# Kernel optimization log

Hardware: AMD Instinct MI355X
Metric: run time of the kernel (lower is better)

The kernel has to match this reference:

```python
import jax, jax.numpy as jnp
import numpy as np
import math

IN_C, OUT_C, KH, KW = 128, 128, 3, 3
GROUPS_NUM, NUM_W = 8, 8
STRIDE, PAD, DIL = 1, 1, 1
BETA = 1.0


def setup_inputs() -> dict:
    key = jax.random.key(0)
    ks = jax.random.split(key, 6)
    B, H, W = 8, 56, 56
    n = IN_C * KH * KW
    bound = math.sqrt(6.0 / n)  # reset_parameters bound for weight templates
    inputs = jax.random.normal(ks[0], (B, IN_C, H, W), jnp.float32)
    mask = jax.random.randint(ks[1], (B, H, W), 0, GROUPS_NUM)
    Alpha = jax.random.uniform(ks[2], (B, GROUPS_NUM, H, W), jnp.float32)
    weight_templates = jax.random.uniform(ks[3], (OUT_C * IN_C * KH * KW, NUM_W), jnp.float32, -bound, bound)
    routing_w = jax.random.normal(ks[4], (GROUPS_NUM * NUM_W, IN_C), jnp.float32) * 0.01
    routing_b = jnp.zeros((GROUPS_NUM * NUM_W,), jnp.float32)
    bias = jnp.zeros((OUT_C,), jnp.float32)
    return dict(inputs=inputs, mask=mask, Alpha=Alpha, weight_templates=weight_templates,
                routing_w=routing_w, routing_b=routing_b, bias=bias, use_alpha=1)


def _unfold(x):
    # torch F.unfold-compatible im2col: [B, C*KH*KW, Ho, Wo], channel-major feature order
    return jax.lax.conv_general_dilated_patches(
        x, (KH, KW), (STRIDE, STRIDE), [(PAD, PAD), (PAD, PAD)],
        rhs_dilation=(DIL, DIL), dimension_numbers=('NCHW', 'OIHW', 'NCHW'))


def reference(inputs, mask, Alpha, weight_templates, routing_w, routing_b, bias, use_alpha):
    B, C, H, W = inputs.shape
    K = IN_C * KH * KW
    # SE-style routing: GAP -> fc -> scaled sigmoid (alpha=1.0 in source)
    x_se = inputs.reshape(B, C, -1).mean(-1)                              # [B, C]
    x_se = 2.0 * jax.nn.sigmoid(x_se @ routing_w.T + routing_b) / NUM_W   # [B, G*num_W]
    # blend weight templates: F.linear(x_se.reshape(-1,num_W), weight)
    w = x_se.reshape(B * GROUPS_NUM, NUM_W) @ weight_templates.T          # [B*G, O*K]
    w = w.reshape(B, GROUPS_NUM, OUT_C, K).transpose(0, 2, 3, 1)          # [B, O, K, G]
    patches = _unfold(inputs)                                             # [B, K, Ho, Wo]
    # per-group convolution outputs, then per-pixel group routing
    y = jnp.einsum('bokg,bkhw->boghw', w, patches)                        # [B, O, G, Ho, Wo]
    if use_alpha:
        probs = jax.nn.softmax(BETA * Alpha, axis=1)                      # soft routing [B, G, Ho, Wo]
    else:
        probs = jax.nn.one_hot(mask, GROUPS_NUM, axis=1, dtype=y.dtype)   # hard per-pixel group select
    out = jnp.einsum('boghw,bghw->bohw', y, probs)
    return out + bias.reshape(1, -1, 1, 1)
```

## Files before the change

kernel.cpp:

```cpp
#include <hip/hip_runtime.h>
#include <stdint.h>

#define IN_C   128
#define OUT_C  128
#define KTOT   1152
#define NG     8
#define NW     8
#define NB     8
#define HH     56
#define WWID   56
#define NPIX   3136
#define PPAD   3200
#define MTOT   1024
#define HALO   58
#define HPIX   (HALO*HALO)


typedef __attribute__((ext_vector_type(8))) short short8;
typedef __attribute__((ext_vector_type(8))) unsigned short ushort8;
typedef __attribute__((ext_vector_type(4))) float f32x4;

__device__ __forceinline__ unsigned short f2bf(float f) {
    unsigned u = __float_as_uint(f);
    u += 0x7FFF + ((u >> 16) & 1);
    return (unsigned short)(u >> 16);
}

__device__ __forceinline__ void cp16(const unsigned short* g, unsigned short* l) {
    __builtin_amdgcn_global_load_lds(
        (const __attribute__((address_space(1))) unsigned int*)g,
        (__attribute__((address_space(3))) unsigned int*)l,
        16, 0, 0);
}

__global__ __launch_bounds__(256) void gap_kernel(const float* __restrict__ in,
                                                  float* __restrict__ xse) {
    const int bc = blockIdx.x;
    const float* src = in + (size_t)bc * NPIX;
    float s = 0.f;
    for (int i = threadIdx.x; i < NPIX / 4; i += 256) {
        float4 v = ((const float4*)src)[i];
        s += v.x + v.y + v.z + v.w;
    }
    #pragma unroll
    for (int off = 32; off; off >>= 1) s += __shfl_down(s, off);
    __shared__ float ws4[4];
    if ((threadIdx.x & 63) == 0) ws4[threadIdx.x >> 6] = s;
    __syncthreads();
    if (threadIdx.x == 0)
        xse[bc] = (ws4[0] + ws4[1] + ws4[2] + ws4[3]) * (1.0f / (float)NPIX);
}

__global__ __launch_bounds__(64) void route_kernel(const float* __restrict__ xse,
                                                   const float* __restrict__ rw,
                                                   const float* __restrict__ rb,
                                                   float* __restrict__ r) {
    const int b = blockIdx.x;
    const int gj = threadIdx.x;
    __shared__ float xs[IN_C];
    xs[gj] = xse[b * IN_C + gj];
    xs[gj + 64] = xse[b * IN_C + 64 + gj];
    __syncthreads();
    float acc = rb[gj];
    #pragma unroll 8
    for (int c = 0; c < IN_C; c++) acc += xs[c] * rw[gj * IN_C + c];
    r[b * 64 + gj] = 0.25f / (1.0f + expf(-acc));
}

__global__ __launch_bounds__(256) void tconv_kernel(const float* __restrict__ T,
                                                    unsigned short* __restrict__ Abf) {
    const int id = blockIdx.x * 256 + threadIdx.x;
    const int m = id / 144;
    const int kc = id - m * 144;
    const int o = m >> 3, j = m & 7;
    const int s = kc >> 4;
    const int c0 = (kc & 15) << 3;
    ushort8 v;
    #pragma unroll
    for (int i = 0; i < 8; i++)
        v[i] = f2bf(T[((size_t)(o * KTOT + (c0 + i) * 9 + s)) * 8 + j]);
    *(ushort8*)&Abf[(size_t)m * KTOT + s * 128 + c0] = v;
}

__global__ __launch_bounds__(256) void transpose_kernel(const float* __restrict__ in,
                                                        unsigned short* __restrict__ Xt) {
    __shared__ unsigned short tile[128 * 128];
    const int t  = threadIdx.x;
    const int yt = blockIdx.x;
    const int b  = blockIdx.y;
    const int y0 = yt * 2;

    #pragma unroll
    for (int it = 0; it < 14; it++) {
        const int f = it * 256 + t;
        const int c = f / 28;
        const int rem = f - c * 28;
        const int y = rem / 14;
        const int x4 = rem - y * 14;
        const float4 v = *(const float4*)(in + ((size_t)(b * IN_C + c)) * NPIX
                                          + (y0 + y) * WWID + x4 * 4);
        unsigned short bf0 = f2bf(v.x), bf1 = f2bf(v.y), bf2 = f2bf(v.z), bf3 = f2bf(v.w);
        const int ppb = (y * WWID + x4 * 4) ^ (((c >> 3) & 15) << 2);
        uint2 pk;
        pk.x = (unsigned)bf0 | ((unsigned)bf1 << 16);
        pk.y = (unsigned)bf2 | ((unsigned)bf3 << 16);
        *(uint2*)&tile[c * 128 + ppb] = pk;
    }
    __syncthreads();

    #pragma unroll
    for (int it = 0; it < 7; it++) {
        const int ch = it * 256 + t;
        const int oct = ch & 15;
        const int pp = ch >> 4;
        const int sw = oct << 2;
        ushort8 v;
        #pragma unroll
        for (int i = 0; i < 8; i++)
            v[i] = tile[(oct * 8 + i) * 128 + (pp ^ sw)];
        const int y2 = (pp >= WWID) ? 1 : 0;
        const int xg = pp - y2 * WWID;
        const size_t hp = (size_t)b * HPIX + (y0 + y2 + 1) * HALO + (xg + 1);
        *(ushort8*)&Xt[hp * 128 + oct * 8] = v;
    }

    if (t < 64) {
        const int pi = t >> 4, oct = t & 15;
        const int yy = y0 + 1 + (pi >> 1);
        const int xx = (pi & 1) * 57;
        *(ushort8*)&Xt[((size_t)b * HPIX + yy * HALO + xx) * 128 + oct * 8] =
            (ushort8){0, 0, 0, 0, 0, 0, 0, 0};
    }
    if (yt == 0 || yt == 27) {
        const int yy = (yt == 0) ? 0 : 57;
        #pragma unroll
        for (int it = 0; it < 4; it++) {
            const int ch = it * 256 + t;
            if (ch < 928) {
                const int xx = ch >> 4, oct = ch & 15;
                *(ushort8*)&Xt[((size_t)b * HPIX + yy * HALO + xx) * 128 + oct * 8] =
                    (ushort8){0, 0, 0, 0, 0, 0, 0, 0};
            }
        }
    }
}

__global__ __launch_bounds__(256) void s_kernel(const float* __restrict__ Alpha,
                                                const int* __restrict__ mask,
                                                const float* __restrict__ r,
                                                const int* __restrict__ use_alpha,
                                                float* __restrict__ Sws) {
    const int b = blockIdx.y;
    const int p = blockIdx.x * 256 + threadIdx.x;
    __shared__ float rsh[64];
    if (threadIdx.x < 64) rsh[threadIdx.x] = r[b * 64 + threadIdx.x];
    __syncthreads();
    if (p >= PPAD) return;
    float sj[8] = {0, 0, 0, 0, 0, 0, 0, 0};
    if (p < NPIX) {
        float pr[8];
        if (use_alpha[0]) {
            float a[8], m = -1e30f;
            #pragma unroll
            for (int g = 0; g < 8; g++) {
                a[g] = Alpha[((size_t)(b * NG + g)) * NPIX + p];
                m = fmaxf(m, a[g]);
            }
            float sum = 0.f;
            #pragma unroll
            for (int g = 0; g < 8; g++) { pr[g] = expf(a[g] - m); sum += pr[g]; }
            float inv = 1.f / sum;
            #pragma unroll
            for (int g = 0; g < 8; g++) pr[g] *= inv;
        } else {
            int mg = mask[(size_t)b * NPIX + p];
            #pragma unroll
            for (int g = 0; g < 8; g++) pr[g] = (g == mg) ? 1.f : 0.f;
        }
        #pragma unroll
        for (int g = 0; g < 8; g++)
            #pragma unroll
            for (int j = 0; j < 8; j++) sj[j] += pr[g] * rsh[g * 8 + j];
    }
    float* dst = Sws + ((size_t)b * PPAD + p) * 8;
    *(f32x4*)dst = (f32x4){sj[0], sj[1], sj[2], sj[3]};
    *(f32x4*)(dst + 4) = (f32x4){sj[4], sj[5], sj[6], sj[7]};
}

__global__ __launch_bounds__(256) void gemm_kernel(const unsigned short* __restrict__ Abf,
                                                   const unsigned short* __restrict__ Xt,
                                                   const float* __restrict__ Sws,
                                                   const float* __restrict__ bias,
                                                   float* __restrict__ out) {
    __shared__ __align__(16) unsigned short Ash[2][512 * 8];
    __shared__ __align__(16) unsigned short Bsh[2][512 * 8];
    const int tid = threadIdx.x;
    const int wv = tid >> 6, ln = tid & 63;
    const int lq = ln >> 4, lr = ln & 15;
    const int wrow = wv >> 1, wcol = wv & 1;

    const int lid = blockIdx.x;
    const int b   = lid & 7;
    const int sl  = lid >> 3;
    const int mt  = sl & 7;
    const int nt  = sl >> 3;

    f32x4 acc[4][4];
    #pragma unroll
    for (int i = 0; i < 4; i++)
        #pragma unroll
        for (int j = 0; j < 4; j++) acc[i][j] = (f32x4){0.f, 0.f, 0.f, 0.f};

    const int r0 = tid >> 2,  q0 = (tid & 3) ^ (r0 & 3);
    const int r1 = r0 + 64,   q1 = (tid & 3) ^ (r1 & 3);
    const unsigned short* ga0 = Abf + (size_t)(mt * 128 + r0) * KTOT + q0 * 8;
    const unsigned short* ga1 = Abf + (size_t)(mt * 128 + r1) * KTOT + q1 * 8;
    const int p0 = min(nt * 128 + r0, NPIX - 1);
    const int p1 = min(nt * 128 + r1, NPIX - 1);
    const int y0p = p0 / WWID, x0p = p0 - y0p * WWID;
    const int y1p = p1 / WWID, x1p = p1 - y1p * WWID;
    const unsigned short* gb0 = Xt + ((size_t)b * HPIX + y0p * HALO + x0p) * 128 + q0 * 8;
    const unsigned short* gb1 = Xt + ((size_t)b * HPIX + y1p * HALO + x1p) * 128 + q1 * 8;

    unsigned short* la0[2] = { &Ash[0][(wv * 64) * 8],       &Ash[1][(wv * 64) * 8] };
    unsigned short* la1[2] = { &Ash[0][(256 + wv * 64) * 8], &Ash[1][(256 + wv * 64) * 8] };
    unsigned short* lb0[2] = { &Bsh[0][(wv * 64) * 8],       &Bsh[1][(wv * 64) * 8] };
    unsigned short* lb1[2] = { &Bsh[0][(256 + wv * 64) * 8], &Bsh[1][(256 + wv * 64) * 8] };

    cp16(ga0, la0[0]); cp16(ga1, la1[0]);
    cp16(gb0, lb0[0]); cp16(gb1, lb1[0]);

    int cur = 0;
    for (int kk = 0; kk < KTOT; kk += 32) {
        __syncthreads();
        const int nk = kk + 32;
        if (nk < KTOT) {
            const int s  = nk >> 7;
            const int kh = s / 3, kw = s - 3 * kh;
            const int offB = (kh * HALO + kw) * 128 + (nk & 127);
            cp16(ga0 + nk, la0[cur ^ 1]); cp16(ga1 + nk, la1[cur ^ 1]);
            cp16(gb0 + offB, lb0[cur ^ 1]); cp16(gb1 + offB, lb1[cur ^ 1]);
        }
        short8 af[4], bfr[4];
        #pragma unroll
        for (int tm = 0; tm < 4; tm++) {
            const int row = wrow * 64 + tm * 16 + lr;
            af[tm] = *(const short8*)&Ash[cur][(row * 4 + (lq ^ (lr & 3))) * 8];
        }
        #pragma unroll
        for (int tn = 0; tn < 4; tn++) {
            const int row = wcol * 64 + tn * 16 + lr;
            bfr[tn] = *(const short8*)&Bsh[cur][(row * 4 + (lq ^ (lr & 3))) * 8];
        }
        #pragma unroll
        for (int tm = 0; tm < 4; tm++)
            #pragma unroll
            for (int tn = 0; tn < 4; tn++)
                acc[tm][tn] = __builtin_amdgcn_mfma_f32_16x16x32_bf16(
                    af[tm], bfr[tn], acc[tm][tn], 0, 0, 0);
        cur ^= 1;
    }

    const int j0 = (lq & 1) * 4;
    const int oo = lq >> 1;
    #pragma unroll
    for (int tm = 0; tm < 4; tm++) {
        const int o = mt * 16 + wrow * 8 + tm * 2 + oo;
        const float bo = bias[o];
        #pragma unroll
        for (int tn = 0; tn < 4; tn++) {
            const int p = nt * 128 + wcol * 64 + tn * 16 + lr;
            const f32x4 sv = *(const f32x4*)&Sws[((size_t)b * PPAD + p) * 8 + j0];
            const f32x4 a = acc[tm][tn];
            float part = a.x * sv.x + a.y * sv.y + a.z * sv.z + a.w * sv.w;
            float tot = part + __shfl_xor(part, 16);
            if ((lq & 1) == 0 && p < NPIX)
                out[((size_t)b * OUT_C + o) * NPIX + p] = tot + bo;
        }
    }
}

extern "C" void kernel_launch(void* const* d_in, const int* in_sizes, int n_in,
                              void* d_out, int out_size, void* d_ws, size_t ws_size,
                              hipStream_t stream) {
    const float* inputs = (const float*)d_in[0];
    const int*   mask   = (const int*)d_in[1];
    const float* Alpha  = (const float*)d_in[2];
    const float* wtmpl  = (const float*)d_in[3];
    const float* rw     = (const float*)d_in[4];
    const float* rb     = (const float*)d_in[5];
    const float* bias   = (const float*)d_in[6];
    const int*   ua     = (const int*)d_in[7];
    float* out = (float*)d_out;

    char* ws = (char*)d_ws;
    unsigned short* Xt  = (unsigned short*)ws;
    unsigned short* Abf = (unsigned short*)(ws + 6889472);
    float*          Sws = (float*)(ws + 9248768);
    float*          xse = (float*)(ws + 10067968);
    float*          rr  = (float*)(ws + 10072064);

    gap_kernel<<<NB * IN_C, 256, 0, stream>>>(inputs, xse);
    route_kernel<<<NB, 64, 0, stream>>>(xse, rw, rb, rr);
    tconv_kernel<<<576, 256, 0, stream>>>(wtmpl, Abf);
    transpose_kernel<<<dim3(28, NB), 256, 0, stream>>>(inputs, Xt);
    s_kernel<<<dim3(13, NB), 256, 0, stream>>>(Alpha, mask, rr, ua, Sws);
    gemm_kernel<<<1600, 256, 0, stream>>>(Abf, Xt, Sws, bias, out);
}
```

Before: 180.3 us.

## Fuse prep kernels and load GEMM A operand directly from global into registers

```diff
diff --git a/kernel.cpp b/kernel.cpp
--- a/kernel.cpp
+++ b/kernel.cpp
@@ -33,61 +33,48 @@
         16, 0, 0);
 }
 
-__global__ __launch_bounds__(256) void gap_kernel(const float* __restrict__ in,
-                                                  float* __restrict__ xse) {
-    const int bc = blockIdx.x;
-    const float* src = in + (size_t)bc * NPIX;
-    float s = 0.f;
-    for (int i = threadIdx.x; i < NPIX / 4; i += 256) {
-        float4 v = ((const float4*)src)[i];
-        s += v.x + v.y + v.z + v.w;
-    }
-    #pragma unroll
-    for (int off = 32; off; off >>= 1) s += __shfl_down(s, off);
-    __shared__ float ws4[4];
-    if ((threadIdx.x & 63) == 0) ws4[threadIdx.x >> 6] = s;
-    __syncthreads();
-    if (threadIdx.x == 0)
-        xse[bc] = (ws4[0] + ws4[1] + ws4[2] + ws4[3]) * (1.0f / (float)NPIX);
-}
-
-__global__ __launch_bounds__(64) void route_kernel(const float* __restrict__ xse,
-                                                   const float* __restrict__ rw,
-                                                   const float* __restrict__ rb,
-                                                   float* __restrict__ r) {
-    const int b = blockIdx.x;
-    const int gj = threadIdx.x;
-    __shared__ float xs[IN_C];
-    xs[gj] = xse[b * IN_C + gj];
-    xs[gj + 64] = xse[b * IN_C + 64 + gj];
-    __syncthreads();
-    float acc = rb[gj];
-    #pragma unroll 8
-    for (int c = 0; c < IN_C; c++) acc += xs[c] * rw[gj * IN_C + c];
-    r[b * 64 + gj] = 0.25f / (1.0f + expf(-acc));
-}
-
-__global__ __launch_bounds__(256) void tconv_kernel(const float* __restrict__ T,
-                                                    unsigned short* __restrict__ Abf) {
-    const int id = blockIdx.x * 256 + threadIdx.x;
-    const int m = id / 144;
-    const int kc = id - m * 144;
-    const int o = m >> 3, j = m & 7;
-    const int s = kc >> 4;
-    const int c0 = (kc & 15) << 3;
-    ushort8 v;
-    #pragma unroll
-    for (int i = 0; i < 8; i++)
-        v[i] = f2bf(T[((size_t)(o * KTOT + (c0 + i) * 9 + s)) * 8 + j]);
-    *(ushort8*)&Abf[(size_t)m * KTOT + s * 128 + c0] = v;
-}
-
-__global__ __launch_bounds__(256) void transpose_kernel(const float* __restrict__ in,
-                                                        unsigned short* __restrict__ Xt) {
+__global__ __launch_bounds__(256) void prep_kernel(const float* __restrict__ in,
+                                                   const float* __restrict__ T,
+                                                   float* __restrict__ xse,
+                                                   unsigned short* __restrict__ Abf,
+                                                   unsigned short* __restrict__ Xt) {
     __shared__ unsigned short tile[128 * 128];
-    const int t  = threadIdx.x;
-    const int yt = blockIdx.x;
-    const int b  = blockIdx.y;
+    const int blk = blockIdx.x;
+    const int t = threadIdx.x;
+
+    if (blk < 1024) {
+        const float* src = in + (size_t)blk * NPIX;
+        float s = 0.f;
+        for (int i = t; i < NPIX / 4; i += 256) {
+            float4 v = ((const float4*)src)[i];
+            s += v.x + v.y + v.z + v.w;
+        }
+        #pragma unroll
+        for (int off = 32; off; off >>= 1) s += __shfl_down(s, off);
+        float* ws4 = (float*)tile;
+        if ((t & 63) == 0) ws4[t >> 6] = s;
+        __syncthreads();
+        if (t == 0)
+            xse[blk] = (ws4[0] + ws4[1] + ws4[2] + ws4[3]) * (1.0f / (float)NPIX);
+        return;
+    }
+    if (blk < 1600) {
+        const int id = (blk - 1024) * 256 + t;
+        const int m = id / 144;
+        const int kc = id - m * 144;
+        const int o = m >> 3, j = m & 7;
+        const int s = kc >> 4;
+        const int c0 = (kc & 15) << 3;
+        ushort8 v;
+        #pragma unroll
+        for (int i = 0; i < 8; i++)
+            v[i] = f2bf(T[((size_t)(o * KTOT + (c0 + i) * 9 + s)) * 8 + j]);
+        *(ushort8*)&Abf[(size_t)m * KTOT + s * 128 + c0] = v;
+        return;
+    }
+    const int idx = blk - 1600;
+    const int yt = idx % 28;
+    const int b  = idx / 28;
     const int y0 = yt * 2;
 
     #pragma unroll
@@ -147,13 +134,24 @@
 
 __global__ __launch_bounds__(256) void s_kernel(const float* __restrict__ Alpha,
                                                 const int* __restrict__ mask,
-                                                const float* __restrict__ r,
+                                                const float* __restrict__ xse,
+                                                const float* __restrict__ rw,
+                                                const float* __restrict__ rb,
                                                 const int* __restrict__ use_alpha,
                                                 float* __restrict__ Sws) {
     const int b = blockIdx.y;
-    const int p = blockIdx.x * 256 + threadIdx.x;
+    const int t = threadIdx.x;
+    const int p = blockIdx.x * 256 + t;
+    __shared__ float xs[IN_C];
     __shared__ float rsh[64];
-    if (threadIdx.x < 64) rsh[threadIdx.x] = r[b * 64 + threadIdx.x];
+    if (t < IN_C) xs[t] = xse[b * IN_C + t];
+    __syncthreads();
+    if (t < 64) {
+        float acc = rb[t];
+        #pragma unroll 8
+        for (int c = 0; c < IN_C; c++) acc += xs[c] * rw[t * IN_C + c];
+        rsh[t] = 0.25f / (1.0f + expf(-acc));
+    }
     __syncthreads();
     if (p >= PPAD) return;
     float sj[8] = {0, 0, 0, 0, 0, 0, 0, 0};
@@ -192,7 +190,6 @@
                                                    const float* __restrict__ Sws,
                                                    const float* __restrict__ bias,
                                                    float* __restrict__ out) {
-    __shared__ __align__(16) unsigned short Ash[2][512 * 8];
     __shared__ __align__(16) unsigned short Bsh[2][512 * 8];
     const int tid = threadIdx.x;
     const int wv = tid >> 6, ln = tid & 63;
@@ -213,52 +210,78 @@
 
     const int r0 = tid >> 2,  q0 = (tid & 3) ^ (r0 & 3);
     const int r1 = r0 + 64,   q1 = (tid & 3) ^ (r1 & 3);
-    const unsigned short* ga0 = Abf + (size_t)(mt * 128 + r0) * KTOT + q0 * 8;
-    const unsigned short* ga1 = Abf + (size_t)(mt * 128 + r1) * KTOT + q1 * 8;
     const int p0 = min(nt * 128 + r0, NPIX - 1);
     const int p1 = min(nt * 128 + r1, NPIX - 1);
     const int y0p = p0 / WWID, x0p = p0 - y0p * WWID;
     const int y1p = p1 / WWID, x1p = p1 - y1p * WWID;
     const unsigned short* gb0 = Xt + ((size_t)b * HPIX + y0p * HALO + x0p) * 128 + q0 * 8;
     const unsigned short* gb1 = Xt + ((size_t)b * HPIX + y1p * HALO + x1p) * 128 + q1 * 8;
-
-    unsigned short* la0[2] = { &Ash[0][(wv * 64) * 8],       &Ash[1][(wv * 64) * 8] };
-    unsigned short* la1[2] = { &Ash[0][(256 + wv * 64) * 8], &Ash[1][(256 + wv * 64) * 8] };
     unsigned short* lb0[2] = { &Bsh[0][(wv * 64) * 8],       &Bsh[1][(wv * 64) * 8] };
     unsigned short* lb1[2] = { &Bsh[0][(256 + wv * 64) * 8], &Bsh[1][(256 + wv * 64) * 8] };
 
-    cp16(ga0, la0[0]); cp16(ga1, la1[0]);
+    const unsigned short* ga[4];
+    #pragma unroll
+    for (int tm = 0; tm < 4; tm++)
+        ga[tm] = Abf + (size_t)(mt * 128 + wrow * 64 + tm * 16 + lr) * KTOT + lq * 8;
+
     cp16(gb0, lb0[0]); cp16(gb1, lb1[0]);
-
-    int cur = 0;
-    for (int kk = 0; kk < KTOT; kk += 32) {
+    short8 afA[4], afB[4];
+    #pragma unroll
+    for (int tm = 0; tm < 4; tm++) afA[tm] = *(const short8*)(ga[tm]);
+
+    #pragma unroll 1
+    for (int it = 0; it < 18; it++) {
+        const int kk = it * 64;
         __syncthreads();
-        const int nk = kk + 32;
-        if (nk < KTOT) {
+        {
+            const int nk = kk + 32;
             const int s  = nk >> 7;
             const int kh = s / 3, kw = s - 3 * kh;
             const int offB = (kh * HALO + kw) * 128 + (nk & 127);
-            cp16(ga0 + nk, la0[cur ^ 1]); cp16(ga1 + nk, la1[cur ^ 1]);
-            cp16(gb0 + offB, lb0[cur ^ 1]); cp16(gb1 + offB, lb1[cur ^ 1]);
-        }
-        short8 af[4], bfr[4];
-        #pragma unroll
-        for (int tm = 0; tm < 4; tm++) {
-            const int row = wrow * 64 + tm * 16 + lr;
-            af[tm] = *(const short8*)&Ash[cur][(row * 4 + (lq ^ (lr & 3))) * 8];
-        }
-        #pragma unroll
-        for (int tn = 0; tn < 4; tn++) {
-            const int row = wcol * 64 + tn * 16 + lr;
-            bfr[tn] = *(const short8*)&Bsh[cur][(row * 4 + (lq ^ (lr & 3))) * 8];
-        }
-        #pragma unroll
-        for (int tm = 0; tm < 4; tm++)
-            #pragma unroll
-            for (int tn = 0; tn < 4; tn++)
-                acc[tm][tn] = __builtin_amdgcn_mfma_f32_16x16x32_bf16(
-                    af[tm], bfr[tn], acc[tm][tn], 0, 0, 0);
-        cur ^= 1;
+            cp16(gb0 + offB, lb0[1]); cp16(gb1 + offB, lb1[1]);
+            #pragma unroll
+            for (int tm = 0; tm < 4; tm++) afB[tm] = *(const short8*)(ga[tm] + nk);
+        }
+        {
+            short8 bfr[4];
+            #pragma unroll
+            for (int tn = 0; tn < 4; tn++) {
+                const int row = wcol * 64 + tn * 16 + lr;
+                bfr[tn] = *(const short8*)&Bsh[0][(row * 4 + (lq ^ (lr & 3))) * 8];
+            }
+            #pragma unroll
+            for (int tm = 0; tm < 4; tm++)
+                #pragma unroll
+                for (int tn = 0; tn < 4; tn++)
+                    acc[tm][tn] = __builtin_amdgcn_mfma_f32_16x16x32_bf16(
+                        afA[tm], bfr[tn], acc[tm][tn], 0, 0, 0);
+        }
+        __syncthreads();
+        {
+            const int nk = kk + 64;
+            if (nk < KTOT) {
+                const int s  = nk >> 7;
+                const int kh = s / 3, kw = s - 3 * kh;
+                const int offB = (kh * HALO + kw) * 128 + (nk & 127);
+                cp16(gb0 + offB, lb0[0]); cp16(gb1 + offB, lb1[0]);
+                #pragma unroll
+                for (int tm = 0; tm < 4; tm++) afA[tm] = *(const short8*)(ga[tm] + nk);
+            }
+        }
+        {
+            short8 bfr[4];
+            #pragma unroll
+            for (int tn = 0; tn < 4; tn++) {
+                const int row = wcol * 64 + tn * 16 + lr;
+                bfr[tn] = *(const short8*)&Bsh[1][(row * 4 + (lq ^ (lr & 3))) * 8];
+            }
+            #pragma unroll
+            for (int tm = 0; tm < 4; tm++)
+                #pragma unroll
+                for (int tn = 0; tn < 4; tn++)
+                    acc[tm][tn] = __builtin_amdgcn_mfma_f32_16x16x32_bf16(
+                        afB[tm], bfr[tn], acc[tm][tn], 0, 0, 0);
+        }
     }
 
     const int j0 = (lq & 1) * 4;
@@ -298,12 +321,8 @@
     unsigned short* Abf = (unsigned short*)(ws + 6889472);
     float*          Sws = (float*)(ws + 9248768);
     float*          xse = (float*)(ws + 10067968);
-    float*          rr  = (float*)(ws + 10072064);
-
-    gap_kernel<<<NB * IN_C, 256, 0, stream>>>(inputs, xse);
-    route_kernel<<<NB, 64, 0, stream>>>(xse, rw, rb, rr);
-    tconv_kernel<<<576, 256, 0, stream>>>(wtmpl, Abf);
-    transpose_kernel<<<dim3(28, NB), 256, 0, stream>>>(inputs, Xt);
-    s_kernel<<<dim3(13, NB), 256, 0, stream>>>(Alpha, mask, rr, ua, Sws);
+
+    prep_kernel<<<1824, 256, 0, stream>>>(inputs, wtmpl, xse, Abf, Xt);
+    s_kernel<<<dim3(13, NB), 256, 0, stream>>>(Alpha, mask, xse, rw, rb, ua, Sws);
     gemm_kernel<<<1600, 256, 0, stream>>>(Abf, Xt, Sws, bias, out);
 }
```

After: 240.2 us. +33.2%, slower.
